# Optimization experiments

Measured on AMD Instinct MI355X. Metric: run time of the kernel, lower is better.

Reference implementation:

```python
import jax, jax.numpy as jnp
import numpy as np

GAMMA = 2.6
SIG0, SIG1 = 0.17, 4.86
EXP_S, EXP_F = 2.0, 0.6

F1_NP = np.array([[0.0025, 0.0125, 0.02, 0.0125, 0.0025],
                  [0.0125, 0.0625, 0.1, 0.0625, 0.0125],
                  [0.02, 0.1, 0.16, 0.1, 0.02],
                  [0.0125, 0.0625, 0.1, 0.0625, 0.0125],
                  [0.0025, 0.0125, 0.02, 0.0125, 0.0025]], dtype=np.float32)[None, None]
FILT0_NP = np.array([[0.04, 0.04, 0.05, 0.04, 0.04],
                     [0.04, 0.03, 0.04, 0.03, 0.04],
                     [0.05, 0.04, 0.05, 0.04, 0.05],
                     [0.04, 0.03, 0.04, 0.03, 0.04],
                     [0.04, 0.04, 0.05, 0.04, 0.04]], dtype=np.float32)[None, None]
FILT1_NP = np.zeros((5, 5), dtype=np.float32)
FILT1_NP[2, 2] = 1.0
FILT1_NP = FILT1_NP[None, None]


def _pad_rep(x, p):
    return jnp.pad(x, ((0, 0), (0, 0), (p, p), (p, p)), mode='edge')


def _conv(x, f, pad=0):
    return jax.lax.conv_general_dilated(
        x, f, window_strides=(1, 1), padding=[(pad, pad), (pad, pad)],
        dimension_numbers=('NCHW', 'OIHW', 'NCHW'))


def _down(img, f):
    # replicate-pad by 2, valid 5x5 conv (output same HxW), stride-2 subsample
    o = _conv(_pad_rep(img, 2), f)
    return o[:, :, ::2, ::2]


def _up(img, odd, f):
    x = _pad_rep(img, 1)
    B, C, Hp, Wp = x.shape
    h, w = 2 * Hp, 2 * Wp
    o = jnp.zeros((B, C, h, w), x.dtype).at[:, :, ::2, ::2].set(4.0 * x)
    o = _conv(o, f, pad=2)
    return o[:, :, 2:h - 2 - odd[0], 2:w - 2 - odd[1]]


def _laplacian_pyramid(img, n_lev, f):
    pyr = []
    o = img
    for _ in range(n_lev - 1):
        g = _down(o, f)
        odd = [g.shape[2] * 2 - o.shape[2], g.shape[3] * 2 - o.shape[3]]
        pyr.append(o - _up(g, odd, f))
        o = g
    pyr.append(o)
    return pyr


def _nlp(img, n_lev, F1, filt0, filt1):
    img = img ** (1.0 / GAMMA)
    pyr = _laplacian_pyramid(img, n_lev, F1)
    npyr = []
    for i in range(n_lev - 1):
        den = _conv(_pad_rep(jnp.abs(pyr[i]), 2), filt0) + SIG0
        npyr.append(pyr[i] / den)
    den = _conv(_pad_rep(jnp.abs(pyr[-1]), 2), filt1) + SIG1
    npyr.append(pyr[-1] / den)
    return npyr


def setup_inputs() -> dict:
    key = jax.random.key(0)
    k1, k2 = jax.random.split(key)
    B, H, W = 16, 512, 512
    h_img = jax.random.uniform(k1, (B, 1, H, W), dtype=jnp.float32)
    l_img = jax.random.uniform(k2, (B, 1, H, W), dtype=jnp.float32)
    return {
        'h_img': h_img,
        'l_img': l_img,
        'F1': jnp.asarray(F1_NP),
        'filt0': jnp.asarray(FILT0_NP),
        'filt1': jnp.asarray(FILT1_NP),
        'n_lev': 7,
    }


def reference(h_img, l_img, F1, filt0, filt1, n_lev):
    h_pyr = _nlp(h_img, n_lev, F1, filt0, filt1)
    l_pyr = _nlp(l_img, n_lev, F1, filt0, filt1)
    dis = []
    for i in range(n_lev):
        diff = jnp.abs(h_pyr[i] - l_pyr[i]) ** EXP_S
        dis.append(jnp.mean(diff, axis=(-2, -1)) ** (EXP_F / EXP_S))  # [B, 1]
    dis = jnp.concatenate(dis, axis=-1)  # [B, n_lev]
    loss = jnp.mean(dis, axis=-1) ** (1.0 / EXP_F)
    return jnp.mean(loss)
```

## Files before the change

kernel.cpp:

```cpp
#include <hip/hip_runtime.h>

#define SIG0 0.17f
#define SIG1 4.86f

__device__ __constant__ float c_filt0[25] = {
  0.04f,0.04f,0.05f,0.04f,0.04f,
  0.04f,0.03f,0.04f,0.03f,0.04f,
  0.05f,0.04f,0.05f,0.04f,0.05f,
  0.04f,0.03f,0.04f,0.03f,0.04f,
  0.04f,0.04f,0.05f,0.04f,0.04f};
__device__ __constant__ float c_f1d[5] = {0.05f,0.25f,0.4f,0.25f,0.05f};

static __device__ __forceinline__ int iclamp(int v, int lo, int hi){
  return v < lo ? lo : (v > hi ? hi : v);
}


struct FS {
  float sg[2][20][76];
  float s1[2][12][44];
  float red[4];
};
struct DS {
  float st[20][136];
  float hs[20][64];
};
struct TS {
  float A3[2][64][66];
  float A4[2][32][34];
  float A5[2][16][18];
  float A6[2][8][10];
  float red[4];
};

__device__ __forceinline__ void down_body(const float* __restrict__ in0, float* __restrict__ out0,
                                          int PSI, int PSO, int Sout, int xo0, int yo0, char* smem){
  DS* S = (DS*)smem;
  int tid = threadIdx.x;
  for (int f=tid; f<20*34; f+=256){
    int r=f/34, c4=f-34*r;
    *(float4*)&S->st[r][4*c4] = *(const float4*)&in0[(size_t)(2*yo0+r)*PSI + 2*xo0 + 4*c4];
  }
  __syncthreads();
  for (int f=tid; f<20*64; f+=256){
    int r=f>>6, xo=f&63;
    const float* rp = &S->st[r][2*xo+2];
    S->hs[r][xo] = 0.05f*rp[0]+0.25f*rp[1]+0.4f*rp[2]+0.25f*rp[3]+0.05f*rp[4];
  }
  __syncthreads();
  for (int f=tid; f<8*64; f+=256){
    int yo=f>>6, xo=f&63;
    int Y=yo0+yo, X=xo0+xo;
    float v = 0.05f*S->hs[2*yo][xo]+0.25f*S->hs[2*yo+1][xo]+0.4f*S->hs[2*yo+2][xo]
            +0.25f*S->hs[2*yo+3][xo]+0.05f*S->hs[2*yo+4][xo];
    int rlo=(Y==0)?0:(Y+2), rhi=(Y==Sout-1)?(Sout+3):(Y+2);
    int clo=(X==0)?0:(X+4), chi=(X==Sout-1)?(Sout+7):(X+4);
    for (int rr=rlo; rr<=rhi; rr++)
      for (int cc=clo; cc<=chi; cc++)
        out0[(size_t)rr*PSO+cc] = v;
  }
}

__global__ __launch_bounds__(256)
void k_d1(const float* __restrict__ hin, const float* __restrict__ lin,
          float* __restrict__ g1){
  __shared__ DS S;
  int xo0 = blockIdx.x*64, yo0 = blockIdx.y*8, z = blockIdx.z;
  const float* in = (z<16)? hin + (size_t)z*262144 : lin + (size_t)(z-16)*262144;
  float* out0 = g1 + (size_t)z*68640;
  int tid = threadIdx.x;
  const float e = 0.3846153846153846f;
  for (int f=tid; f<20*34; f+=256){
    int r=f/34, c4=f-34*r;
    int yy = iclamp(2*yo0-2+r, 0, 511);
    int xb = 2*xo0-4+4*c4;
    const float* rp = in + (size_t)yy*512;
    float4 v;
    if (xb>=0 && xb<=508) v = *(const float4*)&rp[xb];
    else { v.x=rp[iclamp(xb,0,511)]; v.y=rp[iclamp(xb+1,0,511)];
           v.z=rp[iclamp(xb+2,0,511)]; v.w=rp[iclamp(xb+3,0,511)]; }
    v.x=__powf(v.x,e); v.y=__powf(v.y,e); v.z=__powf(v.z,e); v.w=__powf(v.w,e);
    *(float4*)&S.st[r][4*c4] = v;
  }
  __syncthreads();
  for (int f=tid; f<20*64; f+=256){
    int r=f>>6, xo=f&63;
    const float* rp = &S.st[r][2*xo+2];
    S.hs[r][xo] = 0.05f*rp[0]+0.25f*rp[1]+0.4f*rp[2]+0.25f*rp[3]+0.05f*rp[4];
  }
  __syncthreads();
  for (int f=tid; f<8*64; f+=256){
    int yo=f>>6, xo=f&63;
    int Y=yo0+yo, X=xo0+xo;
    float v = 0.05f*S.hs[2*yo][xo]+0.25f*S.hs[2*yo+1][xo]+0.4f*S.hs[2*yo+2][xo]
            +0.25f*S.hs[2*yo+3][xo]+0.05f*S.hs[2*yo+4][xo];
    int rlo=(Y==0)?0:(Y+2), rhi=(Y==255)?259:(Y+2);
    int clo=(X==0)?0:(X+4), chi=(X==255)?263:(X+4);
    for (int rr=rlo; rr<=rhi; rr++)
      for (int cc=clo; cc<=chi; cc++)
        out0[(size_t)rr*264+cc] = v;
  }
}

template<int GAMMA>
__device__ __forceinline__ void fused_body(FS* S,
    const float* __restrict__ a0, const float* __restrict__ a1, int PS0,
    const float* __restrict__ s10, const float* __restrict__ s11, int PS1,
    int Simg, int x0, int y0, float* __restrict__ out_slot){
  int t = threadIdx.x;
  const float e = 0.3846153846153846f;

  if (t < 240){
    int img = t >= 120; int t2 = img ? t-120 : t;
    int r = t2/6, q3 = t2 - 6*r;
    float w[12];
    if (GAMMA){
      int yy = iclamp(y0-2+r, 0, 511);
      int xb = x0-4+12*q3;
      const float* rp = (img ? a1 : a0) + (size_t)yy*512;
      if (xb >= 0 && xb <= 500){
        *(float4*)&w[0] = *(const float4*)&rp[xb];
        *(float4*)&w[4] = *(const float4*)&rp[xb+4];
        *(float4*)&w[8] = *(const float4*)&rp[xb+8];
      } else {
        #pragma unroll
        for (int j=0;j<12;j++) w[j] = rp[iclamp(xb+j,0,511)];
      }
      #pragma unroll
      for (int j=0;j<12;j++) w[j] = __powf(w[j], e);
    } else {
      const float* rp = (img ? a1 : a0) + (size_t)(y0+r)*PS0 + x0 + 12*q3;
      *(float4*)&w[0] = *(const float4*)&rp[0];
      *(float4*)&w[4] = *(const float4*)&rp[4];
      *(float4*)&w[8] = *(const float4*)&rp[8];
    }
    float* dp = &S->sg[img][r][12*q3];
    *(float4*)&dp[0] = *(float4*)&w[0];
    *(float4*)&dp[4] = *(float4*)&w[4];
    *(float4*)&dp[8] = *(float4*)&w[8];
  }
  if (t < 240){
    int img = t >= 120; int t2 = img ? t-120 : t;
    int ro = t2/10, co = t2 - 10*ro;
    const float* src = (img ? s11 : s10) + (size_t)(y0/2+ro)*PS1 + x0/2 + 4*co;
    *(float4*)&S->s1[img][ro][4*co] = *(const float4*)src;
  }
  __syncthreads();

  if (t < 180){
    int img = t >= 90; int t2 = img ? t-90 : t;
    int rp_ = t2/9, q = t2 - 9*rp_;
    int cb1 = 4*q;
    int cbg = 8*q;
    float A[8], B[8], C[8];
    *(float4*)&A[0] = *(const float4*)&S->s1[img][rp_  ][cb1];
    *(float4*)&A[4] = *(const float4*)&S->s1[img][rp_  ][cb1+4];
    *(float4*)&B[0] = *(const float4*)&S->s1[img][rp_+1][cb1];
    *(float4*)&B[4] = *(const float4*)&S->s1[img][rp_+1][cb1+4];
    *(float4*)&C[0] = *(const float4*)&S->s1[img][rp_+2][cb1];
    *(float4*)&C[4] = *(const float4*)&S->s1[img][rp_+2][cb1+4];
    float ue[8], uo[8];
    #pragma unroll
    for (int j=0;j<4;j++){
      float hEA = 0.05f*A[j+1]+0.4f*A[j+2]+0.05f*A[j+3];
      float hEB = 0.05f*B[j+1]+0.4f*B[j+2]+0.05f*B[j+3];
      float hEC = 0.05f*C[j+1]+0.4f*C[j+2]+0.05f*C[j+3];
      float hOA = 0.25f*(A[j+2]+A[j+3]);
      float hOB = 0.25f*(B[j+2]+B[j+3]);
      float hOC = 0.25f*(C[j+2]+C[j+3]);
      ue[2*j]   = 0.2f*hEA + 1.6f*hEB + 0.2f*hEC;
      ue[2*j+1] = 0.2f*hOA + 1.6f*hOB + 0.2f*hOC;
      uo[2*j]   = hEB + hEC;
      uo[2*j+1] = hOB + hOC;
    }
    float* dpe = &S->sg[img][2*rp_][cbg];
    float ve[8];
    *(float4*)&ve[0]=*(float4*)&dpe[0]; *(float4*)&ve[4]=*(float4*)&dpe[4];
    #pragma unroll
    for (int j=0;j<8;j++) ve[j] -= ue[j];
    *(float4*)&dpe[0]=*(float4*)&ve[0]; *(float4*)&dpe[4]=*(float4*)&ve[4];
    float* dpo = &S->sg[img][2*rp_+1][cbg];
    float vo[8];
    *(float4*)&vo[0]=*(float4*)&dpo[0]; *(float4*)&vo[4]=*(float4*)&dpo[4];
    #pragma unroll
    for (int j=0;j<8;j++) vo[j] -= uo[j];
    *(float4*)&dpo[0]=*(float4*)&vo[0]; *(float4*)&dpo[4]=*(float4*)&vo[4];
  }
  __syncthreads();

  bool top=(y0==0), bot=(y0+16==Simg), lft=(x0==0), rgt=(x0+64==Simg);
  if (top|bot|lft|rgt){
    for (int f=t; f<2*18; f+=256){
      int img = f>=18; int q = img ? f-18 : f;
      if (top){ float4 v=*(float4*)&S->sg[img][2][4*q];
                *(float4*)&S->sg[img][0][4*q]=v; *(float4*)&S->sg[img][1][4*q]=v; }
      if (bot){ float4 v=*(float4*)&S->sg[img][17][4*q];
                *(float4*)&S->sg[img][18][4*q]=v; *(float4*)&S->sg[img][19][4*q]=v; }
    }
    __syncthreads();
    for (int f=t; f<2*20; f+=256){
      int img = f>=20; int r = img ? f-20 : f;
      if (lft){ float v=S->sg[img][r][4];  float4 vv={v,v,v,v}; *(float4*)&S->sg[img][r][0]=vv; }
      if (rgt){ float v=S->sg[img][r][67]; float4 vv={v,v,v,v}; *(float4*)&S->sg[img][r][68]=vv; }
    }
    __syncthreads();
  }

  float vacc = 0.f;
  {
    int img = t & 1, quad = t >> 1;
    int qx = quad & 15, qy = quad >> 4;
    int cb = 4*qx, rb = 2*qy;
    float T0[4]={0,0,0,0}, T1[4]={0,0,0,0};
    float s5a[4], s5b[4], s3a[4], s3b[4], n0[4], n1[4];
    #pragma unroll
    for (int r=0;r<6;r++){
      float w[12];
      const float* rp = &S->sg[img][rb+r][cb];
      *(float4*)&w[0]=*(const float4*)&rp[0];
      *(float4*)&w[4]=*(const float4*)&rp[4];
      *(float4*)&w[8]=*(const float4*)&rp[8];
      float aw[8];
      #pragma unroll
      for (int j=0;j<8;j++) aw[j] = fabsf(w[j+2]);
      float h0 = ((aw[0]+aw[1])+(aw[2]+aw[3]))+aw[4];
      float h1 = h0 - aw[0] + aw[5];
      float h2 = h1 - aw[1] + aw[6];
      float h3 = h2 - aw[2] + aw[7];
      float hh[4] = {h0,h1,h2,h3};
      if (r<=4){
        #pragma unroll
        for (int c=0;c<4;c++) T0[c] += hh[c];
      }
      if (r>=1){
        #pragma unroll
        for (int c=0;c<4;c++) T1[c] += hh[c];
      }
      if (r==0){
        for (int c=0;c<4;c++) s5a[c] = aw[c+2];
      }
      if (r==1){
        for (int c=0;c<4;c++){ s3a[c] = aw[c+1]+aw[c+3]; s5b[c] = aw[c+2]; }
      }
      if (r==2){
        for (int c=0;c<4;c++){ s5a[c] += aw[c]+aw[c+2]+aw[c+4]; n0[c]=w[c+4]; s3b[c] = aw[c+1]+aw[c+3]; }
      }
      if (r==3){
        for (int c=0;c<4;c++){ s3a[c] += aw[c+1]+aw[c+3]; s5b[c] += aw[c]+aw[c+2]+aw[c+4]; n1[c]=w[c+4]; }
      }
      if (r==4){
        for (int c=0;c<4;c++){ s5a[c] += aw[c+2]; s3b[c] += aw[c+1]+aw[c+3]; }
      }
      if (r==5){
        for (int c=0;c<4;c++) s5b[c] += aw[c+2];
      }
    }
    float qv[8];
    #pragma unroll
    for (int c=0;c<4;c++){
      float d0 = SIG0 + 0.04f*T0[c] + 0.01f*s5a[c] - 0.01f*s3a[c];
      float d1 = SIG0 + 0.04f*T1[c] + 0.01f*s5b[c] - 0.01f*s3b[c];
      qv[c]   = __fdividef(n0[c], d0);
      qv[4+c] = __fdividef(n1[c], d1);
    }
    #pragma unroll
    for (int i=0;i<8;i++){
      float o = __shfl_xor(qv[i], 1);
      float d = qv[i] - o;
      vacc += d*d;
    }
    if (img) vacc = 0.f;
  }
  #pragma unroll
  for (int off=32; off>0; off>>=1) vacc += __shfl_down(vacc, off);
  if ((t&63)==0) S->red[t>>6] = vacc;
  __syncthreads();
  if (t==0)
    out_slot[0] = S->red[0]+S->red[1]+S->red[2]+S->red[3];
}

static __device__ __forceinline__ void down_lds(const float* Ain, int ldi, int Sin,
                                                float* Aout, int ldo, int Sout,
                                                int tid, int NT){
  int tot = 2*Sout*Sout;
  for (int f=tid; f<tot; f+=NT){
    int img = f/(Sout*Sout), rem = f%(Sout*Sout), y=rem/Sout, x=rem%Sout;
    const float* A = Ain + img*Sin*ldi;
    float s=0.f;
    #pragma unroll
    for (int i=0;i<5;i++){
      int yy=iclamp(2*y+i-2,0,Sin-1);
      float rs=0.f;
      #pragma unroll
      for (int j=0;j<5;j++){
        int xx=iclamp(2*x+j-2,0,Sin-1);
        rs += c_f1d[j]*A[yy*ldi+xx];
      }
      s += c_f1d[i]*rs;
    }
    Aout[img*Sout*ldo + y*ldo + x] = s;
  }
}

static __device__ __forceinline__ void lap_lds(float* Ak, int ldk, int S,
                                               const float* Ag, int ldg,
                                               int tid, int NT){
  int Sg = S>>1;
  int tot = 2*S*S;
  for (int f=tid; f<tot; f+=NT){
    int img=f/(S*S), rem=f%(S*S), y=rem/S, x=rem%S;
    const float* G = Ag + img*Sg*ldg;
    int y2=y>>1, x2=x>>1;
    int ry0,ry1,ry2; float wy0,wy1,wy2;
    if (!(y&1)){ ry0=iclamp(y2-1,0,Sg-1); ry1=y2; ry2=iclamp(y2+1,0,Sg-1); wy0=0.2f; wy1=1.6f; wy2=0.2f; }
    else { ry0=y2; ry1=iclamp(y2+1,0,Sg-1); ry2=y2; wy0=1.f; wy1=1.f; wy2=0.f; }
    int cx0,cx1,cx2; float wx0,wx1,wx2;
    if (!(x&1)){ cx0=iclamp(x2-1,0,Sg-1); cx1=x2; cx2=iclamp(x2+1,0,Sg-1); wx0=0.05f; wx1=0.4f; wx2=0.05f; }
    else { cx0=x2; cx1=iclamp(x2+1,0,Sg-1); cx2=x2; wx0=0.25f; wx1=0.25f; wx2=0.f; }
    float u0 = wx0*G[ry0*ldg+cx0]+wx1*G[ry0*ldg+cx1]+wx2*G[ry0*ldg+cx2];
    float u1 = wx0*G[ry1*ldg+cx0]+wx1*G[ry1*ldg+cx1]+wx2*G[ry1*ldg+cx2];
    float u2 = wx0*G[ry2*ldg+cx0]+wx1*G[ry2*ldg+cx1]+wx2*G[ry2*ldg+cx2];
    Ak[img*S*ldk + y*ldk + x] -= wy0*u0+wy1*u1+wy2*u2;
  }
}

static __device__ __forceinline__ float diff_lds(const float* A, int ld, int S,
                                                 int tid, int NT){
  float v=0.f;
  const float* Ah = A;
  const float* Al = A + S*ld;
  for (int f=tid; f<S*S; f+=NT){
    int y=f/S, x=f%S;
    float dh=SIG0, dl=SIG0;
    #pragma unroll
    for (int i=0;i<5;i++){
      int yy=iclamp(y+i-2,0,S-1);
      #pragma unroll
      for (int j=0;j<5;j++){
        int xx=iclamp(x+j-2,0,S-1);
        float w=c_filt0[i*5+j];
        dh += w*fabsf(Ah[yy*ld+xx]);
        dl += w*fabsf(Al[yy*ld+xx]);
      }
    }
    float d = __fdividef(Ah[y*ld+x],dh) - __fdividef(Al[y*ld+x],dl);
    v += d*d;
  }
  return v;
}

__device__ void tail_body(const float* __restrict__ g3, float* __restrict__ accum,
                          int b, char* smem){
  TS* T = (TS*)smem;
  int tid = threadIdx.x;
  const float* s0  = g3 + (size_t)b*4896 + 148;
  const float* s1p = g3 + (size_t)(b+16)*4896 + 148;
  for (int f=tid; f<2*4096; f+=256){
    int img=f>>12, rem=f&4095, r=rem>>6, c=rem&63;
    T->A3[img][r][c] = (img? s1p : s0)[(size_t)r*72+c];
  }
  __syncthreads();
  down_lds(&T->A3[0][0][0],66,64,&T->A4[0][0][0],34,32,tid,256);
  __syncthreads();
  down_lds(&T->A4[0][0][0],34,32,&T->A5[0][0][0],18,16,tid,256);
  __syncthreads();
  down_lds(&T->A5[0][0][0],18,16,&T->A6[0][0][0],10,8,tid,256);
  __syncthreads();
  lap_lds(&T->A3[0][0][0],66,64,&T->A4[0][0][0],34,tid,256);
  __syncthreads();
  float v3 = diff_lds(&T->A3[0][0][0],66,64,tid,256);
  lap_lds(&T->A4[0][0][0],34,32,&T->A5[0][0][0],18,tid,256);
  __syncthreads();
  float v4 = diff_lds(&T->A4[0][0][0],34,32,tid,256);
  lap_lds(&T->A5[0][0][0],18,16,&T->A6[0][0][0],10,tid,256);
  __syncthreads();
  float v5 = diff_lds(&T->A5[0][0][0],18,16,tid,256);
  float v6 = 0.f;
  for (int f=tid; f<64; f+=256){
    float ch = T->A6[0][f>>3][f&7];
    float cl = T->A6[1][f>>3][f&7];
    float d = __fdividef(ch, fabsf(ch)+SIG1) - __fdividef(cl, fabsf(cl)+SIG1);
    v6 += d*d;
  }
  float vs[4] = {v3, v4, v5, v6};
  #pragma unroll
  for (int k=0;k<4;k++){
    float v = vs[k];
    #pragma unroll
    for (int off=32; off>0; off>>=1) v += __shfl_down(v, off);
    if ((tid&63)==0) T->red[tid>>6] = v;
    __syncthreads();
    if (tid==0)
      accum[(3+k)*16 + b] = T->red[0]+T->red[1]+T->red[2]+T->red[3];
    __syncthreads();
  }
}

__global__ __launch_bounds__(256)
void k_fused0(const float* __restrict__ h, const float* __restrict__ l,
              const float* __restrict__ g1, float* __restrict__ p0){
  extern __shared__ char smem[];
  int b = blockIdx.z, x0 = blockIdx.x*64, y0 = blockIdx.y*16;
  fused_body<1>((FS*)smem, h+(size_t)b*262144, l+(size_t)b*262144, 0,
                g1+(size_t)b*68640, g1+(size_t)(b+16)*68640, 264,
                512, x0, y0, p0 + b*256 + blockIdx.y*8 + blockIdx.x);
}

__global__ __launch_bounds__(256)
void k_down1(const float* __restrict__ g1, float* __restrict__ g2){
  extern __shared__ char smem[];
  down_body(g1+(size_t)blockIdx.z*68640, g2+(size_t)blockIdx.z*17952, 264, 136, 128,
            blockIdx.x*64, blockIdx.y*8, smem);
}

__global__ __launch_bounds__(256)
void k_d4(const float* __restrict__ g1, float* __restrict__ g2,
          float* __restrict__ g3, float* __restrict__ p1){
  extern __shared__ char smem[];
  if (blockIdx.z < 16){
    int b = blockIdx.z, x0 = blockIdx.x*64, y0 = blockIdx.y*16;
    fused_body<0>((FS*)smem, g1+(size_t)b*68640, g1+(size_t)(b+16)*68640, 264,
                  g2+(size_t)b*17952, g2+(size_t)(b+16)*17952, 136,
                  256, x0, y0, p1 + b*64 + blockIdx.y*4 + blockIdx.x);
  } else {
    int id = (blockIdx.z-16)*64 + blockIdx.y*4 + blockIdx.x;
    int img = id>>3, yt = id&7;
    down_body(g2+(size_t)img*17952, g3+(size_t)img*4896, 136, 72, 64, 0, yt*8, smem);
  }
}

__global__ __launch_bounds__(256)
void k_d5(const float* __restrict__ g2, const float* __restrict__ g3,
          float* __restrict__ p2, float* __restrict__ accum){
  extern __shared__ char smem[];
  if (blockIdx.z < 16){
    int b = blockIdx.z, x0 = blockIdx.x*64, y0 = blockIdx.y*16;
    fused_body<0>((FS*)smem, g2+(size_t)b*17952, g2+(size_t)(b+16)*17952, 136,
                  g3+(size_t)b*4896, g3+(size_t)(b+16)*4896, 72,
                  128, x0, y0, p2 + b*16 + blockIdx.y*2 + blockIdx.x);
  } else {
    int id = blockIdx.y*2 + blockIdx.x;
    tail_body(g3, accum, id, smem);
  }
}

__global__ __launch_bounds__(256)
void k_d6(const float* __restrict__ p0, const float* __restrict__ p1,
          const float* __restrict__ p2, const float* __restrict__ accum,
          float* __restrict__ out){
  __shared__ float r0[16][16];
  __shared__ float r1[16][4];
  __shared__ float r2[16];
  __shared__ float fin[16];
  int t = threadIdx.x;
  {
    int b = t>>4, c = t&15;
    float s = 0.f;
    #pragma unroll
    for (int j=0;j<16;j++) s += p0[b*256 + c*16 + j];
    r0[b][c] = s;
  }
  if (t < 64){
    int b = t>>2, c = t&3;
    float s = 0.f;
    #pragma unroll
    for (int j=0;j<16;j++) s += p1[b*64 + c*16 + j];
    r1[b][c] = s;
  }
  if (t < 16){
    float s = 0.f;
    #pragma unroll
    for (int j=0;j<16;j++) s += p2[t*16 + j];
    r2[t] = s;
  }
  __syncthreads();
  if (t < 16){
    int b = t;
    float a0 = 0.f;
    #pragma unroll
    for (int c=0;c<16;c++) a0 += r0[b][c];
    float a1 = (r1[b][0]+r1[b][1])+(r1[b][2]+r1[b][3]);
    float a2 = r2[b];
    float m = powf(a0*(1.0f/262144.0f), 0.3f)
            + powf(a1*(1.0f/65536.0f), 0.3f)
            + powf(a2*(1.0f/16384.0f), 0.3f);
    #pragma unroll
    for (int k=3;k<7;k++){
      int hw = (512>>k)*(512>>k);
      m += powf(accum[k*16+b]/(float)hw, 0.3f);
    }
    m *= (1.0f/7.0f);
    fin[b] = powf(m, 1.6666666666666667f);
  }
  __syncthreads();
  if (t == 0){
    float s = 0.f;
    #pragma unroll
    for (int i=0;i<16;i++) s += fin[i];
    out[0] = s * (1.0f/16.0f);
  }
}

extern "C" void kernel_launch(void* const* d_in, const int* in_sizes, int n_in,
                              void* d_out, int out_size, void* d_ws, size_t ws_size,
                              hipStream_t stream){
  const float* h = (const float*)d_in[0];
  const float* l = (const float*)d_in[1];
  float* out = (float*)d_out;
  float* ws = (float*)d_ws;

  float* g1 = ws;
  float* g2 = g1 + 2196480;
  float* g3 = g2 + 574464;
  float* accum = g3 + 156672;
  float* p0 = accum + 112;
  float* p1 = p0 + 4096;
  float* p2 = p1 + 1024;

  size_t fsz = sizeof(FS) > sizeof(DS) ? sizeof(FS) : sizeof(DS);
  size_t tsz = sizeof(TS);

  k_d1<<<dim3(4,32,32), 256, 0, stream>>>(h, l, g1);
  k_fused0<<<dim3(8,32,16), 256, sizeof(FS), stream>>>(h, l, g1, p0);
  k_down1<<<dim3(2,16,32), 256, sizeof(DS), stream>>>(g1, g2);
  k_d4<<<dim3(4,16,20), 256, fsz, stream>>>(g1, g2, g3, p1);
  k_d5<<<dim3(2,8,17),  256, tsz, stream>>>(g2, g3, p2, accum);
  k_d6<<<1, 256, 0, stream>>>(p0, p1, p2, accum, out);
}
```

Baseline: 163.0 us.

## Retile pyramid kernels to full-row strips and split merged launches into separate kernels

Downsample and fused Laplacian/normalisation kernels now use wide row strips (full image width at the coarser levels) instead of 64-wide tiles, with tile sizes set by template parameters. This cuts halo overhead and the number of blocks. The previously merged heterogeneous launches (fused plus down plus tail in one grid) become separate kernels: k_down<256>, k_fused1, k_down<128>, k_fused2 and k_tail. The aim is less redundant halo loading and simpler per-block work, at the cost of more kernel launches and fewer, larger blocks at the coarse levels, which may underfill the GPU.

```diff
diff --git a/kernel.cpp b/kernel.cpp
--- a/kernel.cpp
+++ b/kernel.cpp
@@ -14,86 +14,49 @@
 static __device__ __forceinline__ int iclamp(int v, int lo, int hi){
   return v < lo ? lo : (v > hi ? hi : v);
 }
-
-
-struct FS {
-  float sg[2][20][76];
-  float s1[2][12][44];
-  float red[4];
-};
-struct DS {
-  float st[20][136];
-  float hs[20][64];
-};
-struct TS {
-  float A3[2][64][66];
-  float A4[2][32][34];
-  float A5[2][16][18];
-  float A6[2][8][10];
-  float red[4];
-};
-
-__device__ __forceinline__ void down_body(const float* __restrict__ in0, float* __restrict__ out0,
-                                          int PSI, int PSO, int Sout, int xo0, int yo0, char* smem){
-  DS* S = (DS*)smem;
-  int tid = threadIdx.x;
-  for (int f=tid; f<20*34; f+=256){
-    int r=f/34, c4=f-34*r;
-    *(float4*)&S->st[r][4*c4] = *(const float4*)&in0[(size_t)(2*yo0+r)*PSI + 2*xo0 + 4*c4];
-  }
-  __syncthreads();
-  for (int f=tid; f<20*64; f+=256){
-    int r=f>>6, xo=f&63;
-    const float* rp = &S->st[r][2*xo+2];
-    S->hs[r][xo] = 0.05f*rp[0]+0.25f*rp[1]+0.4f*rp[2]+0.25f*rp[3]+0.05f*rp[4];
-  }
-  __syncthreads();
-  for (int f=tid; f<8*64; f+=256){
-    int yo=f>>6, xo=f&63;
-    int Y=yo0+yo, X=xo0+xo;
-    float v = 0.05f*S->hs[2*yo][xo]+0.25f*S->hs[2*yo+1][xo]+0.4f*S->hs[2*yo+2][xo]
-            +0.25f*S->hs[2*yo+3][xo]+0.05f*S->hs[2*yo+4][xo];
-    int rlo=(Y==0)?0:(Y+2), rhi=(Y==Sout-1)?(Sout+3):(Y+2);
-    int clo=(X==0)?0:(X+4), chi=(X==Sout-1)?(Sout+7):(X+4);
-    for (int rr=rlo; rr<=rhi; rr++)
-      for (int cc=clo; cc<=chi; cc++)
-        out0[(size_t)rr*PSO+cc] = v;
-  }
-}
+static __device__ __forceinline__ float4 gamma4(float4 v){
+  const float e = 0.3846153846153846f;
+  v.x = __powf(v.x, e); v.y = __powf(v.y, e);
+  v.z = __powf(v.z, e); v.w = __powf(v.w, e);
+  return v;
+}
+
 
 __global__ __launch_bounds__(256)
 void k_d1(const float* __restrict__ hin, const float* __restrict__ lin,
           float* __restrict__ g1){
-  __shared__ DS S;
-  int xo0 = blockIdx.x*64, yo0 = blockIdx.y*8, z = blockIdx.z;
+  extern __shared__ float sm[];
+  float* ST = sm;
+  float* HS = sm + 20*520;
+  int bx = blockIdx.x, z = blockIdx.y;
   const float* in = (z<16)? hin + (size_t)z*262144 : lin + (size_t)(z-16)*262144;
   float* out0 = g1 + (size_t)z*68640;
-  int tid = threadIdx.x;
-  const float e = 0.3846153846153846f;
-  for (int f=tid; f<20*34; f+=256){
-    int r=f/34, c4=f-34*r;
-    int yy = iclamp(2*yo0-2+r, 0, 511);
-    int xb = 2*xo0-4+4*c4;
-    const float* rp = in + (size_t)yy*512;
-    float4 v;
-    if (xb>=0 && xb<=508) v = *(const float4*)&rp[xb];
-    else { v.x=rp[iclamp(xb,0,511)]; v.y=rp[iclamp(xb+1,0,511)];
-           v.z=rp[iclamp(xb+2,0,511)]; v.w=rp[iclamp(xb+3,0,511)]; }
-    v.x=__powf(v.x,e); v.y=__powf(v.y,e); v.z=__powf(v.z,e); v.w=__powf(v.w,e);
-    *(float4*)&S.st[r][4*c4] = v;
-  }
-  __syncthreads();
-  for (int f=tid; f<20*64; f+=256){
-    int r=f>>6, xo=f&63;
-    const float* rp = &S.st[r][2*xo+2];
-    S.hs[r][xo] = 0.05f*rp[0]+0.25f*rp[1]+0.4f*rp[2]+0.25f*rp[3]+0.05f*rp[4];
-  }
-  __syncthreads();
-  for (int f=tid; f<8*64; f+=256){
-    int yo=f>>6, xo=f&63;
-    int Y=yo0+yo, X=xo0+xo;
-    float v = 0.05f*S.hs[2*yo][xo]+0.25f*S.hs[2*yo+1][xo]+0.4f*S.hs[2*yo+2][xo]
-            +0.25f*S.hs[2*yo+3][xo]+0.05f*S.hs[2*yo+4][xo];
+  int t = threadIdx.x;
+  for (int f=t; f<2560; f+=256){
+    int r = f>>7, ch = f&127;
+    int yy = iclamp(16*bx-2+r, 0, 511);
+    float4 v = *(const float4*)&in[(size_t)yy*512 + 4*ch];
+    *(float4*)&ST[r*520 + 4 + 4*ch] = gamma4(v);
+  }
+  __syncthreads();
+  if (t < 20){
+    float vl = ST[t*520 + 4],  vr = ST[t*520 + 515];
+    float4 v4l = {vl,vl,vl,vl}, v4r = {vr,vr,vr,vr};
+    *(float4*)&ST[t*520 + 0]   = v4l;
+    *(float4*)&ST[t*520 + 516] = v4r;
+  }
+  __syncthreads();
+  for (int f=t; f<5120; f+=256){
+    int r = f>>8, xo = f&255;
+    const float* rp = &ST[r*520 + 2*xo + 2];
+    HS[r*256 + xo] = 0.05f*rp[0]+0.25f*rp[1]+0.4f*rp[2]+0.25f*rp[3]+0.05f*rp[4];
+  }
+  __syncthreads();
+  for (int f=t; f<2048; f+=256){
+    int yo = f>>8, X = f&255;
+    int Y = 8*bx + yo;
+    float v = 0.05f*HS[(2*yo)*256+X]+0.25f*HS[(2*yo+1)*256+X]+0.4f*HS[(2*yo+2)*256+X]
+            +0.25f*HS[(2*yo+3)*256+X]+0.05f*HS[(2*yo+4)*256+X];
     int rlo=(Y==0)?0:(Y+2), rhi=(Y==255)?259:(Y+2);
     int clo=(X==0)?0:(X+4), chi=(X==255)?263:(X+4);
     for (int rr=rlo; rr<=rhi; rr++)
@@ -102,63 +65,109 @@
   }
 }
 
-template<int GAMMA>
-__device__ __forceinline__ void fused_body(FS* S,
-    const float* __restrict__ a0, const float* __restrict__ a1, int PS0,
-    const float* __restrict__ s10, const float* __restrict__ s11, int PS1,
-    int Simg, int x0, int y0, float* __restrict__ out_slot){
+template<int SIN>
+__global__ __launch_bounds__(256)
+void k_down(const float* __restrict__ gin, float* __restrict__ gout){
+  constexpr int WI = SIN+8, SO = SIN/2, PO = SO+8;
+  constexpr int CH = WI/4;
+  extern __shared__ float sm[];
+  float* ST = sm;
+  float* HS = sm + 20*WI;
+  int bx = blockIdx.x, z = blockIdx.y;
+  const float* in0 = gin + (size_t)z * (size_t)((SIN+4)*WI);
+  float* out0 = gout + (size_t)z * (size_t)((SO+4)*PO);
   int t = threadIdx.x;
-  const float e = 0.3846153846153846f;
-
-  if (t < 240){
-    int img = t >= 120; int t2 = img ? t-120 : t;
-    int r = t2/6, q3 = t2 - 6*r;
-    float w[12];
-    if (GAMMA){
-      int yy = iclamp(y0-2+r, 0, 511);
-      int xb = x0-4+12*q3;
-      const float* rp = (img ? a1 : a0) + (size_t)yy*512;
-      if (xb >= 0 && xb <= 500){
-        *(float4*)&w[0] = *(const float4*)&rp[xb];
-        *(float4*)&w[4] = *(const float4*)&rp[xb+4];
-        *(float4*)&w[8] = *(const float4*)&rp[xb+8];
-      } else {
-        #pragma unroll
-        for (int j=0;j<12;j++) w[j] = rp[iclamp(xb+j,0,511)];
-      }
-      #pragma unroll
-      for (int j=0;j<12;j++) w[j] = __powf(w[j], e);
-    } else {
-      const float* rp = (img ? a1 : a0) + (size_t)(y0+r)*PS0 + x0 + 12*q3;
-      *(float4*)&w[0] = *(const float4*)&rp[0];
-      *(float4*)&w[4] = *(const float4*)&rp[4];
-      *(float4*)&w[8] = *(const float4*)&rp[8];
-    }
-    float* dp = &S->sg[img][r][12*q3];
-    *(float4*)&dp[0] = *(float4*)&w[0];
-    *(float4*)&dp[4] = *(float4*)&w[4];
-    *(float4*)&dp[8] = *(float4*)&w[8];
-  }
-  if (t < 240){
-    int img = t >= 120; int t2 = img ? t-120 : t;
-    int ro = t2/10, co = t2 - 10*ro;
-    const float* src = (img ? s11 : s10) + (size_t)(y0/2+ro)*PS1 + x0/2 + 4*co;
-    *(float4*)&S->s1[img][ro][4*co] = *(const float4*)src;
-  }
-  __syncthreads();
-
-  if (t < 180){
-    int img = t >= 90; int t2 = img ? t-90 : t;
-    int rp_ = t2/9, q = t2 - 9*rp_;
-    int cb1 = 4*q;
-    int cbg = 8*q;
+  for (int f=t; f<20*CH; f+=256){
+    int r = f/CH, ch = f - r*CH;
+    *(float4*)&ST[r*WI + 4*ch] = *(const float4*)&in0[(size_t)(16*bx + r)*WI + 4*ch];
+  }
+  __syncthreads();
+  for (int f=t; f<20*SO; f+=256){
+    int r = f/SO, xo = f - r*SO;
+    const float* rp = &ST[r*WI + 2*xo + 2];
+    HS[r*SO + xo] = 0.05f*rp[0]+0.25f*rp[1]+0.4f*rp[2]+0.25f*rp[3]+0.05f*rp[4];
+  }
+  __syncthreads();
+  for (int f=t; f<8*SO; f+=256){
+    int yo = f/SO, X = f - yo*SO;
+    int Y = 8*bx + yo;
+    float v = 0.05f*HS[(2*yo)*SO+X]+0.25f*HS[(2*yo+1)*SO+X]+0.4f*HS[(2*yo+2)*SO+X]
+            +0.25f*HS[(2*yo+3)*SO+X]+0.05f*HS[(2*yo+4)*SO+X];
+    int rlo=(Y==0)?0:(Y+2), rhi=(Y==SO-1)?(SO+3):(Y+2);
+    int clo=(X==0)?0:(X+4), chi=(X==SO-1)?(SO+7):(X+4);
+    for (int rr=rlo; rr<=rhi; rr++)
+      for (int cc=clo; cc<=chi; cc++)
+        out0[(size_t)rr*PO+cc] = v;
+  }
+}
+
+template<int GAMMA, int SIMG, int TW, int TH>
+__device__ __forceinline__ void fused_body(
+    const float* __restrict__ a0, const float* __restrict__ a1,
+    const float* __restrict__ s10, const float* __restrict__ s11,
+    int xt, int yt, float* __restrict__ out_slot)
+{
+  constexpr int WL  = TW + 8;
+  constexpr int W1L = TW/2 + 8;
+  constexpr int PS1 = SIMG/2 + 8;
+  constexpr int NR  = TH + 4;
+  constexpr int NR1 = TH/2 + 4;
+  constexpr int PRS = NR/2;
+  constexpr int NSEG= WL/8;
+  constexpr int NQX = TW/4;
+  constexpr int LQX = (NQX==64)?6:5;
+  constexpr int QY  = TH/2;
+  constexpr int CH  = WL/4;
+  constexpr int CH1 = W1L/4;
+  extern __shared__ float sm[];
+  float* SG  = sm;
+  float* S1L = sm + 2*NR*WL;
+  float* RED = S1L + 2*NR1*W1L;
+  const int t = threadIdx.x;
+  const int x0 = TW*xt, y0 = TH*yt;
+
+  if (GAMMA){
+    for (int f=t; f<2*NR*CH; f+=256){
+      int img = f >= NR*CH; int rem = img ? f - NR*CH : f;
+      int rr = rem/CH, ch = rem - rr*CH;
+      int yy = iclamp(y0-2+rr, 0, SIMG-1);
+      int xb = x0 - 4 + 4*ch;
+      const float* rp = (img ? a1 : a0) + (size_t)yy*SIMG;
+      float4 v;
+      if (xb >= 0 && xb <= SIMG-4) v = *(const float4*)&rp[xb];
+      else { v.x=rp[iclamp(xb,0,SIMG-1)]; v.y=rp[iclamp(xb+1,0,SIMG-1)];
+             v.z=rp[iclamp(xb+2,0,SIMG-1)]; v.w=rp[iclamp(xb+3,0,SIMG-1)]; }
+      *(float4*)&SG[(img*NR+rr)*WL + 4*ch] = gamma4(v);
+    }
+  } else {
+    for (int f=t; f<2*NR*CH; f+=256){
+      int img = f >= NR*CH; int rem = img ? f - NR*CH : f;
+      int rr = rem/CH, ch = rem - rr*CH;
+      const float* src = img ? a1 : a0;
+      *(float4*)&SG[(img*NR+rr)*WL + 4*ch] =
+          *(const float4*)&src[(size_t)(y0+rr)*WL + 4*ch];
+    }
+  }
+  for (int f=t; f<2*NR1*CH1; f+=256){
+    int img = f >= NR1*CH1; int rem = img ? f - NR1*CH1 : f;
+    int ro = rem/CH1, ch = rem - ro*CH1;
+    const float* src = img ? s11 : s10;
+    *(float4*)&S1L[(img*NR1+ro)*W1L + 4*ch] =
+        *(const float4*)&src[(size_t)(y0/2+ro)*PS1 + x0/2 + 4*ch];
+  }
+  __syncthreads();
+
+  for (int f=t; f<2*PRS*NSEG; f+=256){
+    int img = f >= PRS*NSEG; int rem = img ? f - PRS*NSEG : f;
+    int p = rem/NSEG, q = rem - p*NSEG;
+    const float* s1b = S1L + img*NR1*W1L;
     float A[8], B[8], C[8];
-    *(float4*)&A[0] = *(const float4*)&S->s1[img][rp_  ][cb1];
-    *(float4*)&A[4] = *(const float4*)&S->s1[img][rp_  ][cb1+4];
-    *(float4*)&B[0] = *(const float4*)&S->s1[img][rp_+1][cb1];
-    *(float4*)&B[4] = *(const float4*)&S->s1[img][rp_+1][cb1+4];
-    *(float4*)&C[0] = *(const float4*)&S->s1[img][rp_+2][cb1];
-    *(float4*)&C[4] = *(const float4*)&S->s1[img][rp_+2][cb1+4];
+    { const float* pr = s1b + p*W1L + 4*q;
+      *(float4*)&A[0]=*(const float4*)&pr[0]; *(float4*)&A[4]=*(const float4*)&pr[4]; }
+    { const float* pr = s1b + (p+1)*W1L + 4*q;
+      *(float4*)&B[0]=*(const float4*)&pr[0]; *(float4*)&B[4]=*(const float4*)&pr[4]; }
+    { const float* pr = s1b + (p+2)*W1L + 4*q;
+      *(float4*)&C[0]=*(const float4*)&pr[0]; *(float4*)&C[4]=*(const float4*)&pr[4]; }
     float ue[8], uo[8];
     #pragma unroll
     for (int j=0;j<4;j++){
@@ -173,50 +182,59 @@
       uo[2*j]   = hEB + hEC;
       uo[2*j+1] = hOB + hOC;
     }
-    float* dpe = &S->sg[img][2*rp_][cbg];
-    float ve[8];
-    *(float4*)&ve[0]=*(float4*)&dpe[0]; *(float4*)&ve[4]=*(float4*)&dpe[4];
-    #pragma unroll
-    for (int j=0;j<8;j++) ve[j] -= ue[j];
-    *(float4*)&dpe[0]=*(float4*)&ve[0]; *(float4*)&dpe[4]=*(float4*)&ve[4];
-    float* dpo = &S->sg[img][2*rp_+1][cbg];
-    float vo[8];
-    *(float4*)&vo[0]=*(float4*)&dpo[0]; *(float4*)&vo[4]=*(float4*)&dpo[4];
-    #pragma unroll
-    for (int j=0;j<8;j++) vo[j] -= uo[j];
-    *(float4*)&dpo[0]=*(float4*)&vo[0]; *(float4*)&dpo[4]=*(float4*)&vo[4];
-  }
-  __syncthreads();
-
-  bool top=(y0==0), bot=(y0+16==Simg), lft=(x0==0), rgt=(x0+64==Simg);
-  if (top|bot|lft|rgt){
-    for (int f=t; f<2*18; f+=256){
-      int img = f>=18; int q = img ? f-18 : f;
-      if (top){ float4 v=*(float4*)&S->sg[img][2][4*q];
-                *(float4*)&S->sg[img][0][4*q]=v; *(float4*)&S->sg[img][1][4*q]=v; }
-      if (bot){ float4 v=*(float4*)&S->sg[img][17][4*q];
-                *(float4*)&S->sg[img][18][4*q]=v; *(float4*)&S->sg[img][19][4*q]=v; }
-    }
-    __syncthreads();
-    for (int f=t; f<2*20; f+=256){
-      int img = f>=20; int r = img ? f-20 : f;
-      if (lft){ float v=S->sg[img][r][4];  float4 vv={v,v,v,v}; *(float4*)&S->sg[img][r][0]=vv; }
-      if (rgt){ float v=S->sg[img][r][67]; float4 vv={v,v,v,v}; *(float4*)&S->sg[img][r][68]=vv; }
-    }
-    __syncthreads();
-  }
+    float* re = SG + (img*NR + 2*p)*WL + 8*q;
+    float* ro_ = SG + (img*NR + 2*p+1)*WL + 8*q;
+    float ve[8], vo[8];
+    *(float4*)&ve[0]=*(float4*)&re[0]; *(float4*)&ve[4]=*(float4*)&re[4];
+    *(float4*)&vo[0]=*(float4*)&ro_[0]; *(float4*)&vo[4]=*(float4*)&ro_[4];
+    #pragma unroll
+    for (int j=0;j<8;j++){ ve[j] -= ue[j]; vo[j] -= uo[j]; }
+    *(float4*)&re[0]=*(float4*)&ve[0]; *(float4*)&re[4]=*(float4*)&ve[4];
+    *(float4*)&ro_[0]=*(float4*)&vo[0]; *(float4*)&ro_[4]=*(float4*)&vo[4];
+  }
+  __syncthreads();
+
+  {
+    bool top = (y0 == 0), bot = (y0 + TH == SIMG);
+    if (top | bot){
+      for (int f=t; f<2*CH; f+=256){
+        int img = f >= CH; int ch = img ? f - CH : f;
+        float* base = SG + img*NR*WL;
+        if (top){ float4 v = *(float4*)&base[2*WL + 4*ch];
+          *(float4*)&base[0*WL + 4*ch] = v; *(float4*)&base[1*WL + 4*ch] = v; }
+        if (bot){ float4 v = *(float4*)&base[(TH+1)*WL + 4*ch];
+          *(float4*)&base[(TH+2)*WL + 4*ch] = v; *(float4*)&base[(TH+3)*WL + 4*ch] = v; }
+      }
+    }
+  }
+  __syncthreads();
+  {
+    bool lft = (x0 == 0), rgt = (x0 + TW == SIMG);
+    if ((lft | rgt) && t < 2*NR){
+      int img = t >= NR; int r = img ? t - NR : t;
+      float* row = SG + (img*NR + r)*WL;
+      if (lft){ float v = row[4];    float4 v4 = {v,v,v,v}; *(float4*)&row[0]    = v4; }
+      if (rgt){ float v = row[WL-5]; float4 v4 = {v,v,v,v}; *(float4*)&row[WL-4] = v4; }
+    }
+  }
+  __syncthreads();
 
   float vacc = 0.f;
-  {
-    int img = t & 1, quad = t >> 1;
-    int qx = quad & 15, qy = quad >> 4;
+  constexpr int P3N = 2*NQX*QY;
+  for (int k=0; k<P3N/256; k++){
+    int u = t + 256*k;
+    int img = u & 1;
+    int quad = u >> 1;
+    int qx = quad & (NQX-1);
+    int qy = quad >> LQX;
+    const float* sgb = SG + img*NR*WL;
     int cb = 4*qx, rb = 2*qy;
     float T0[4]={0,0,0,0}, T1[4]={0,0,0,0};
     float s5a[4], s5b[4], s3a[4], s3b[4], n0[4], n1[4];
     #pragma unroll
     for (int r=0;r<6;r++){
       float w[12];
-      const float* rp = &S->sg[img][rb+r][cb];
+      const float* rp = &sgb[(rb+r)*WL + cb];
       *(float4*)&w[0]=*(const float4*)&rp[0];
       *(float4*)&w[4]=*(const float4*)&rp[4];
       *(float4*)&w[8]=*(const float4*)&rp[8];
@@ -269,15 +287,48 @@
       float d = qv[i] - o;
       vacc += d*d;
     }
-    if (img) vacc = 0.f;
-  }
+  }
+  if (t & 1) vacc = 0.f;
   #pragma unroll
   for (int off=32; off>0; off>>=1) vacc += __shfl_down(vacc, off);
-  if ((t&63)==0) S->red[t>>6] = vacc;
+  if ((t&63)==0) RED[t>>6] = vacc;
   __syncthreads();
   if (t==0)
-    out_slot[0] = S->red[0]+S->red[1]+S->red[2]+S->red[3];
-}
+    out_slot[0] = RED[0]+RED[1]+RED[2]+RED[3];
+}
+
+__global__ __launch_bounds__(256)
+void k_fused0(const float* __restrict__ h, const float* __restrict__ l,
+              const float* __restrict__ g1, float* __restrict__ p0){
+  int xt = blockIdx.x, yt = blockIdx.y, z = blockIdx.z;
+  fused_body<1,512,256,16>(h + (size_t)z*262144, l + (size_t)z*262144,
+                           g1 + (size_t)z*68640, g1 + (size_t)(z+16)*68640,
+                           xt, yt, p0 + z*64 + yt*2 + xt);
+}
+__global__ __launch_bounds__(256)
+void k_fused1(const float* __restrict__ g1, const float* __restrict__ g2,
+              float* __restrict__ p1){
+  int yt = blockIdx.x, z = blockIdx.y;
+  fused_body<0,256,256,8>(g1 + (size_t)z*68640, g1 + (size_t)(z+16)*68640,
+                          g2 + (size_t)z*17952, g2 + (size_t)(z+16)*17952,
+                          0, yt, p1 + z*32 + yt);
+}
+__global__ __launch_bounds__(256)
+void k_fused2(const float* __restrict__ g2, const float* __restrict__ g3,
+              float* __restrict__ p2s){
+  int yt = blockIdx.x, z = blockIdx.y;
+  fused_body<0,128,128,8>(g2 + (size_t)z*17952, g2 + (size_t)(z+16)*17952,
+                          g3 + (size_t)z*4896, g3 + (size_t)(z+16)*4896,
+                          0, yt, p2s + z*16 + yt);
+}
+
+struct TS {
+  float A3[2][64][66];
+  float A4[2][32][34];
+  float A5[2][16][18];
+  float A6[2][8][10];
+  float red[4];
+};
 
 static __device__ __forceinline__ void down_lds(const float* Ain, int ldi, int Sin,
                                                 float* Aout, int ldo, int Sout,
@@ -301,7 +352,6 @@
     Aout[img*Sout*ldo + y*ldo + x] = s;
   }
 }
-
 static __device__ __forceinline__ void lap_lds(float* Ak, int ldk, int S,
                                                const float* Ag, int ldg,
                                                int tid, int NT){
@@ -323,7 +373,6 @@
     Ak[img*S*ldk + y*ldk + x] -= wy0*u0+wy1*u1+wy2*u2;
   }
 }
-
 static __device__ __forceinline__ float diff_lds(const float* A, int ld, int S,
                                                  int tid, int NT){
   float v=0.f;
@@ -349,9 +398,11 @@
   return v;
 }
 
-__device__ void tail_body(const float* __restrict__ g3, float* __restrict__ accum,
-                          int b, char* smem){
+__global__ __launch_bounds__(256)
+void k_tail(const float* __restrict__ g3, float* __restrict__ accum){
+  extern __shared__ char smem[];
   TS* T = (TS*)smem;
+  int b = blockIdx.x;
   int tid = threadIdx.x;
   const float* s0  = g3 + (size_t)b*4896 + 148;
   const float* s1p = g3 + (size_t)(b+16)*4896 + 148;
@@ -396,101 +447,27 @@
   }
 }
 
-__global__ __launch_bounds__(256)
-void k_fused0(const float* __restrict__ h, const float* __restrict__ l,
-              const float* __restrict__ g1, float* __restrict__ p0){
-  extern __shared__ char smem[];
-  int b = blockIdx.z, x0 = blockIdx.x*64, y0 = blockIdx.y*16;
-  fused_body<1>((FS*)smem, h+(size_t)b*262144, l+(size_t)b*262144, 0,
-                g1+(size_t)b*68640, g1+(size_t)(b+16)*68640, 264,
-                512, x0, y0, p0 + b*256 + blockIdx.y*8 + blockIdx.x);
-}
-
-__global__ __launch_bounds__(256)
-void k_down1(const float* __restrict__ g1, float* __restrict__ g2){
-  extern __shared__ char smem[];
-  down_body(g1+(size_t)blockIdx.z*68640, g2+(size_t)blockIdx.z*17952, 264, 136, 128,
-            blockIdx.x*64, blockIdx.y*8, smem);
-}
-
-__global__ __launch_bounds__(256)
-void k_d4(const float* __restrict__ g1, float* __restrict__ g2,
-          float* __restrict__ g3, float* __restrict__ p1){
-  extern __shared__ char smem[];
-  if (blockIdx.z < 16){
-    int b = blockIdx.z, x0 = blockIdx.x*64, y0 = blockIdx.y*16;
-    fused_body<0>((FS*)smem, g1+(size_t)b*68640, g1+(size_t)(b+16)*68640, 264,
-                  g2+(size_t)b*17952, g2+(size_t)(b+16)*17952, 136,
-                  256, x0, y0, p1 + b*64 + blockIdx.y*4 + blockIdx.x);
-  } else {
-    int id = (blockIdx.z-16)*64 + blockIdx.y*4 + blockIdx.x;
-    int img = id>>3, yt = id&7;
-    down_body(g2+(size_t)img*17952, g3+(size_t)img*4896, 136, 72, 64, 0, yt*8, smem);
-  }
-}
-
-__global__ __launch_bounds__(256)
-void k_d5(const float* __restrict__ g2, const float* __restrict__ g3,
-          float* __restrict__ p2, float* __restrict__ accum){
-  extern __shared__ char smem[];
-  if (blockIdx.z < 16){
-    int b = blockIdx.z, x0 = blockIdx.x*64, y0 = blockIdx.y*16;
-    fused_body<0>((FS*)smem, g2+(size_t)b*17952, g2+(size_t)(b+16)*17952, 136,
-                  g3+(size_t)b*4896, g3+(size_t)(b+16)*4896, 72,
-                  128, x0, y0, p2 + b*16 + blockIdx.y*2 + blockIdx.x);
-  } else {
-    int id = blockIdx.y*2 + blockIdx.x;
-    tail_body(g3, accum, id, smem);
-  }
-}
-
-__global__ __launch_bounds__(256)
+__global__ __launch_bounds__(64)
 void k_d6(const float* __restrict__ p0, const float* __restrict__ p1,
-          const float* __restrict__ p2, const float* __restrict__ accum,
+          const float* __restrict__ p2s, const float* __restrict__ accum,
           float* __restrict__ out){
-  __shared__ float r0[16][16];
-  __shared__ float r1[16][4];
-  __shared__ float r2[16];
   __shared__ float fin[16];
   int t = threadIdx.x;
-  {
-    int b = t>>4, c = t&15;
-    float s = 0.f;
-    #pragma unroll
-    for (int j=0;j<16;j++) s += p0[b*256 + c*16 + j];
-    r0[b][c] = s;
-  }
-  if (t < 64){
-    int b = t>>2, c = t&3;
-    float s = 0.f;
-    #pragma unroll
-    for (int j=0;j<16;j++) s += p1[b*64 + c*16 + j];
-    r1[b][c] = s;
-  }
   if (t < 16){
-    float s = 0.f;
-    #pragma unroll
-    for (int j=0;j<16;j++) s += p2[t*16 + j];
-    r2[t] = s;
-  }
-  __syncthreads();
-  if (t < 16){
-    int b = t;
-    float a0 = 0.f;
-    #pragma unroll
-    for (int c=0;c<16;c++) a0 += r0[b][c];
-    float a1 = (r1[b][0]+r1[b][1])+(r1[b][2]+r1[b][3]);
-    float a2 = r2[b];
+    float a0=0.f, a1=0.f, a2=0.f;
+    for (int j=0;j<64;j++) a0 += p0[t*64+j];
+    for (int j=0;j<32;j++) a1 += p1[t*32+j];
+    for (int j=0;j<16;j++) a2 += p2s[t*16+j];
     float m = powf(a0*(1.0f/262144.0f), 0.3f)
             + powf(a1*(1.0f/65536.0f), 0.3f)
             + powf(a2*(1.0f/16384.0f), 0.3f);
     #pragma unroll
     for (int k=3;k<7;k++){
       int hw = (512>>k)*(512>>k);
-      m += powf(accum[k*16+b]/(float)hw, 0.3f);
+      m += powf(accum[k*16+t]/(float)hw, 0.3f);
     }
     m *= (1.0f/7.0f);
-    fin[b] = powf(m, 1.6666666666666667f);
+    fin[t] = powf(m, 1.6666666666666667f);
   }
   __syncthreads();
   if (t == 0){
@@ -514,16 +491,22 @@
   float* g3 = g2 + 574464;
   float* accum = g3 + 156672;
   float* p0 = accum + 112;
-  float* p1 = p0 + 4096;
-  float* p2 = p1 + 1024;
-
-  size_t fsz = sizeof(FS) > sizeof(DS) ? sizeof(FS) : sizeof(DS);
-  size_t tsz = sizeof(TS);
-
-  k_d1<<<dim3(4,32,32), 256, 0, stream>>>(h, l, g1);
-  k_fused0<<<dim3(8,32,16), 256, sizeof(FS), stream>>>(h, l, g1, p0);
-  k_down1<<<dim3(2,16,32), 256, sizeof(DS), stream>>>(g1, g2);
-  k_d4<<<dim3(4,16,20), 256, fsz, stream>>>(g1, g2, g3, p1);
-  k_d5<<<dim3(2,8,17),  256, tsz, stream>>>(g2, g3, p2, accum);
-  k_d6<<<1, 256, 0, stream>>>(p0, p1, p2, accum, out);
-}
+  float* p1 = p0 + 1024;
+  float* p2s = p1 + 512;
+
+  const size_t ld1  = (20*520 + 20*256)*sizeof(float);
+  const size_t lf0  = (2*20*264 + 2*12*136 + 4)*sizeof(float);
+  const size_t ldn1 = (20*264 + 20*128)*sizeof(float);
+  const size_t lf1  = (2*12*264 + 2*8*136 + 4)*sizeof(float);
+  const size_t ldn2 = (20*136 + 20*64)*sizeof(float);
+  const size_t lf2  = (2*12*136 + 2*8*72 + 4)*sizeof(float);
+
+  k_d1        <<<dim3(32,32),   256, ld1,  stream>>>(h, l, g1);
+  k_fused0    <<<dim3(2,32,16), 256, lf0,  stream>>>(h, l, g1, p0);
+  k_down<256> <<<dim3(16,32),   256, ldn1, stream>>>(g1, g2);
+  k_fused1    <<<dim3(32,16),   256, lf1,  stream>>>(g1, g2, p1);
+  k_down<128> <<<dim3(8,32),    256, ldn2, stream>>>(g2, g3);
+  k_fused2    <<<dim3(16,16),   256, lf2,  stream>>>(g2, g3, p2s);
+  k_tail      <<<16, 256, sizeof(TS), stream>>>(g3, accum);
+  k_d6        <<<1, 64, 0, stream>>>(p0, p1, p2s, accum, out);
+}
```

New measurement: 187.6 us. 15.1% more time.

## Merge level-0 fused kernel with level-1 downsample and widen per-thread output tile

Applied to the files above, without the earlier changes.

Folds the k_fused0 and k_down1 launches into one kernel, k_d2, which uses extra grid z-slices to run the downsample blocks next to the level-0 fused blocks. This removes one launch and lets the two independent workloads share the GPU at once. Separately, the per-thread normalisation stage now computes 4 output rows instead of 2, with only 128 threads active, so overlapping 5-row windows reuse more LDS reads. The cost is higher register pressure and half the threads sitting idle in that stage.

```diff
diff --git a/kernel.cpp b/kernel.cpp
--- a/kernel.cpp
+++ b/kernel.cpp
@@ -207,19 +207,26 @@
   }
 
   float vacc = 0.f;
-  {
+  if (t < 128){
     int img = t & 1, quad = t >> 1;
     int qx = quad & 15, qy = quad >> 4;
-    int cb = 4*qx, rb = 2*qy;
-    float T0[4]={0,0,0,0}, T1[4]={0,0,0,0};
-    float s5a[4], s5b[4], s3a[4], s3b[4], n0[4], n1[4];
-    #pragma unroll
-    for (int r=0;r<6;r++){
+    int cb = 4*qx, rb = 4*qy;
+    float T[4][4], s5[4][4], s3[4][4], n[4][4];
+    #pragma unroll
+    for (int o=0;o<4;o++){
+      #pragma unroll
+      for (int c=0;c<4;c++){ T[o][c]=0.f; s5[o][c]=0.f; s3[o][c]=0.f; }
+    }
+    #pragma unroll
+    for (int r=0;r<8;r++){
+      const float* rp = &S->sg[img][rb+r][cb];
+      float4 t0 = *(const float4*)&rp[0];
+      float4 t1 = *(const float4*)&rp[4];
+      float4 t2 = *(const float4*)&rp[8];
       float w[12];
-      const float* rp = &S->sg[img][rb+r][cb];
-      *(float4*)&w[0]=*(const float4*)&rp[0];
-      *(float4*)&w[4]=*(const float4*)&rp[4];
-      *(float4*)&w[8]=*(const float4*)&rp[8];
+      w[0]=t0.x; w[1]=t0.y; w[2]=t0.z;  w[3]=t0.w;
+      w[4]=t1.x; w[5]=t1.y; w[6]=t1.z;  w[7]=t1.w;
+      w[8]=t2.x; w[9]=t2.y; w[10]=t2.z; w[11]=t2.w;
       float aw[8];
       #pragma unroll
       for (int j=0;j<8;j++) aw[j] = fabsf(w[j+2]);
@@ -228,46 +235,36 @@
       float h2 = h1 - aw[1] + aw[6];
       float h3 = h2 - aw[2] + aw[7];
       float hh[4] = {h0,h1,h2,h3};
-      if (r<=4){
-        #pragma unroll
-        for (int c=0;c<4;c++) T0[c] += hh[c];
+      #pragma unroll
+      for (int o=0;o<4;o++){
+        if (r>=o && r<=o+4){
+          #pragma unroll
+          for (int c=0;c<4;c++) T[o][c] += hh[c];
+        }
+        if (r==o || r==o+4){
+          #pragma unroll
+          for (int c=0;c<4;c++) s5[o][c] += aw[c+2];
+        }
+        if (r==o+2){
+          #pragma unroll
+          for (int c=0;c<4;c++){ s5[o][c] += aw[c]+aw[c+2]+aw[c+4]; n[o][c] = w[c+4]; }
+        }
+        if (r==o+1 || r==o+3){
+          #pragma unroll
+          for (int c=0;c<4;c++) s3[o][c] += aw[c+1]+aw[c+3];
+        }
       }
-      if (r>=1){
-        #pragma unroll
-        for (int c=0;c<4;c++) T1[c] += hh[c];
+    }
+    #pragma unroll
+    for (int o=0;o<4;o++){
+      #pragma unroll
+      for (int c=0;c<4;c++){
+        float den = SIG0 + 0.04f*T[o][c] + 0.01f*s5[o][c] - 0.01f*s3[o][c];
+        float qv = __fdividef(n[o][c], den);
+        float other = __shfl_xor(qv, 1);
+        float d = qv - other;
+        vacc += d*d;
       }
-      if (r==0){
-        for (int c=0;c<4;c++) s5a[c] = aw[c+2];
-      }
-      if (r==1){
-        for (int c=0;c<4;c++){ s3a[c] = aw[c+1]+aw[c+3]; s5b[c] = aw[c+2]; }
-      }
-      if (r==2){
-        for (int c=0;c<4;c++){ s5a[c] += aw[c]+aw[c+2]+aw[c+4]; n0[c]=w[c+4]; s3b[c] = aw[c+1]+aw[c+3]; }
-      }
-      if (r==3){
-        for (int c=0;c<4;c++){ s3a[c] += aw[c+1]+aw[c+3]; s5b[c] += aw[c]+aw[c+2]+aw[c+4]; n1[c]=w[c+4]; }
-      }
-      if (r==4){
-        for (int c=0;c<4;c++){ s5a[c] += aw[c+2]; s3b[c] += aw[c+1]+aw[c+3]; }
-      }
-      if (r==5){
-        for (int c=0;c<4;c++) s5b[c] += aw[c+2];
-      }
-    }
-    float qv[8];
-    #pragma unroll
-    for (int c=0;c<4;c++){
-      float d0 = SIG0 + 0.04f*T0[c] + 0.01f*s5a[c] - 0.01f*s3a[c];
-      float d1 = SIG0 + 0.04f*T1[c] + 0.01f*s5b[c] - 0.01f*s3b[c];
-      qv[c]   = __fdividef(n0[c], d0);
-      qv[4+c] = __fdividef(n1[c], d1);
-    }
-    #pragma unroll
-    for (int i=0;i<8;i++){
-      float o = __shfl_xor(qv[i], 1);
-      float d = qv[i] - o;
-      vacc += d*d;
     }
     if (img) vacc = 0.f;
   }
@@ -397,20 +394,20 @@
 }
 
 __global__ __launch_bounds__(256)
-void k_fused0(const float* __restrict__ h, const float* __restrict__ l,
-              const float* __restrict__ g1, float* __restrict__ p0){
+void k_d2(const float* __restrict__ h, const float* __restrict__ l,
+          const float* __restrict__ g1, float* __restrict__ g2,
+          float* __restrict__ p0){
   extern __shared__ char smem[];
-  int b = blockIdx.z, x0 = blockIdx.x*64, y0 = blockIdx.y*16;
-  fused_body<1>((FS*)smem, h+(size_t)b*262144, l+(size_t)b*262144, 0,
-                g1+(size_t)b*68640, g1+(size_t)(b+16)*68640, 264,
-                512, x0, y0, p0 + b*256 + blockIdx.y*8 + blockIdx.x);
-}
-
-__global__ __launch_bounds__(256)
-void k_down1(const float* __restrict__ g1, float* __restrict__ g2){
-  extern __shared__ char smem[];
-  down_body(g1+(size_t)blockIdx.z*68640, g2+(size_t)blockIdx.z*17952, 264, 136, 128,
-            blockIdx.x*64, blockIdx.y*8, smem);
+  if (blockIdx.z < 16){
+    int b = blockIdx.z, x0 = blockIdx.x*64, y0 = blockIdx.y*16;
+    fused_body<1>((FS*)smem, h+(size_t)b*262144, l+(size_t)b*262144, 0,
+                  g1+(size_t)b*68640, g1+(size_t)(b+16)*68640, 264,
+                  512, x0, y0, p0 + b*256 + blockIdx.y*8 + blockIdx.x);
+  } else {
+    int id = (blockIdx.z-16)*256 + blockIdx.y*8 + blockIdx.x;
+    int img = id>>5, rem = id&31, xt = rem&1, yt = rem>>1;
+    down_body(g1+(size_t)img*68640, g2+(size_t)img*17952, 264, 136, 128, xt*64, yt*8, smem);
+  }
 }
 
 __global__ __launch_bounds__(256)
@@ -521,8 +518,7 @@
   size_t tsz = sizeof(TS);
 
   k_d1<<<dim3(4,32,32), 256, 0, stream>>>(h, l, g1);
-  k_fused0<<<dim3(8,32,16), 256, sizeof(FS), stream>>>(h, l, g1, p0);
-  k_down1<<<dim3(2,16,32), 256, sizeof(DS), stream>>>(g1, g2);
+  k_d2<<<dim3(8,32,20), 256, fsz, stream>>>(h, l, g1, g2, p0);
   k_d4<<<dim3(4,16,20), 256, fsz, stream>>>(g1, g2, g3, p1);
   k_d5<<<dim3(2,8,17),  256, tsz, stream>>>(g2, g3, p2, accum);
   k_d6<<<1, 256, 0, stream>>>(p0, p1, p2, accum, out);
```

Result: faster. 159.2 us (-2.3%).
